# Kernel tuning notes

Measured on AMD Instinct MI355X. Metric: run time of the kernel, lower is better.

The kernel has to match this reference:

```python
import jax, jax.numpy as jnp
import numpy as np

EPS = 0.05      # entropic regularization, matches eps arg in forward
ITERS = 100     # Sinkhorn fixed-point iterations (auction analog; converged math)

def setup_inputs() -> dict:
    key = jax.random.key(0)
    k1, k2 = jax.random.split(key)
    B, N, D = 16, 2048, 3
    x = jax.random.uniform(k1, (B, N, D), dtype=jnp.float32)
    y = jax.random.uniform(k2, (B, N, D), dtype=jnp.float32)
    return {"x": x, "y": y}

def _emd_mean(x, y):
    # pairwise squared distances: [B, N, N]
    x2 = jnp.sum(x * x, axis=-1)                      # [B, N]
    y2 = jnp.sum(y * y, axis=-1)                      # [B, N]
    xy = jnp.einsum('bnd,bmd->bnm', x, y)             # [B, N, N]
    C = x2[:, :, None] + y2[:, None, :] - 2.0 * xy
    C = jnp.maximum(C, 0.0)

    B, N, _ = C.shape
    logK = -C / EPS                                   # [B, N, N]
    log_mu = jnp.full((B, N), -jnp.log(jnp.float32(N)))
    log_nu = log_mu

    def body(carry, _):
        f, g = carry
        # f_i = eps*(log mu_i - logsumexp_j((g_j - C_ij)/eps))
        f = EPS * (log_mu - jax.nn.logsumexp(logK + (g / EPS)[:, None, :], axis=2))
        g = EPS * (log_nu - jax.nn.logsumexp(logK + (f / EPS)[:, :, None], axis=1))
        return (f, g), None

    f0 = jnp.zeros((B, N), dtype=C.dtype)
    g0 = jnp.zeros((B, N), dtype=C.dtype)
    (f, g), _ = jax.lax.scan(body, (f0, g0), None, length=ITERS)

    # transport plan P_ij = exp((f_i + g_j - C_ij)/eps) (already includes mu,nu)
    logP = (f[:, :, None] + g[:, None, :] - C) / EPS
    P = jnp.exp(logP)
    # per-source-point matched squared distance, scaled by N (row mass = 1/N)
    dis = jnp.sum(P * C, axis=2) * N                  # [B, N]
    return dis.mean()

def reference(x, y):
    return _emd_mean(x, y)
```

## Files before the change

kernel.cpp:

```cpp
#include <hip/hip_runtime.h>

#define BB 16
#define NN 2048
#define NITERS 100

#define K2E      28.853900817779268f
#define TWO_K2E  57.707801635558536f
#define INV2K    0.017328679513998632f
#define INV_K2E  0.034657359027997264f
#define INV4K    0.008664339756999316f
#define LMU      (-11.0f)

#if __has_builtin(__builtin_amdgcn_exp2f)
#define EXP2F(x) __builtin_amdgcn_exp2f(x)
#else
#define EXP2F(x) exp2f(x)
#endif

typedef float v2f __attribute__((ext_vector_type(2)));
typedef float v4f __attribute__((ext_vector_type(4)));

#define DSTORE(p, v) __hip_atomic_store((p), (v), __ATOMIC_RELAXED, __HIP_MEMORY_SCOPE_AGENT)
#define DLOAD(p)     __hip_atomic_load((p), __ATOMIC_RELAXED, __HIP_MEMORY_SCOPE_AGENT)

__device__ __forceinline__ float bfly8(const float acc[8], int lane) {
    const bool b0 = lane & 1, b1 = lane & 2, b2 = lane & 4;
    float v4[4], v2_[2], v1;
    #pragma unroll
    for (int i = 0; i < 4; ++i) {
        float recv = __shfl_xor(b0 ? acc[i] : acc[i+4], 1, 64);
        v4[i] = (b0 ? acc[i+4] : acc[i]) + recv;
    }
    #pragma unroll
    for (int i = 0; i < 2; ++i) {
        float recv = __shfl_xor(b1 ? v4[i] : v4[i+2], 2, 64);
        v2_[i] = (b1 ? v4[i+2] : v4[i]) + recv;
    }
    {
        float recv = __shfl_xor(b2 ? v2_[0] : v2_[1], 4, 64);
        v1 = (b2 ? v2_[1] : v2_[0]) + recv;
    }
    v1 += __shfl_xor(v1, 8, 64);
    v1 += __shfl_xor(v1, 16, 64);
    v1 += __shfl_xor(v1, 32, 64);
    return v1;
}

__device__ __forceinline__ float sumpassF(
    const v4f* __restrict__ U, const v4f* __restrict__ T,
    const float* __restrict__ sdv,
    int rloc, int lane)
{
    v2f xp0[4], xp1[4], xp2[4], acc2[4];
    #pragma unroll
    for (int p = 0; p < 4; ++p) {
        const v4f ua = U[rloc + 2*p];
        const v4f ub = U[rloc + 2*p + 1];
        xp0[p] = (v2f){ua.x * INV2K, ub.x * INV2K};
        xp1[p] = (v2f){ua.y * INV2K, ub.y * INV2K};
        xp2[p] = (v2f){ua.z * INV2K, ub.z * INV2K};
        acc2[p] = (v2f){0.f, 0.f};
    }
    #pragma unroll 4
    for (int s = 0; s < 32; ++s) {
        const int p = lane + (s << 6);
        const v4f t = T[p];
        const float ad = sdv[p];
        const v2f a0v = (v2f){t.x, t.x}, a1v = (v2f){t.y, t.y};
        const v2f a2v = (v2f){t.z, t.z}, adv = (v2f){ad, ad};
        #pragma unroll
        for (int qq = 0; qq < 4; ++qq) {
            v2f d = __builtin_elementwise_fma(xp0[qq], a0v,
                    __builtin_elementwise_fma(xp1[qq], a1v,
                    __builtin_elementwise_fma(xp2[qq], a2v, adv)));
            acc2[qq] += (v2f){EXP2F(d.x), EXP2F(d.y)};
        }
    }
    float acc[8];
    #pragma unroll
    for (int p = 0; p < 4; ++p) { acc[2*p] = acc2[p].x; acc[2*p+1] = acc2[p].y; }
    return bfly8(acc, lane);
}

__device__ __forceinline__ float epilA(
    const v4f* __restrict__ U, const v4f* __restrict__ T,
    const float* __restrict__ gB,
    float Aval, int rloc, int jh, int lane)
{
    const int jb = (jh << 10) + lane;
    float dv[16];
    #pragma unroll
    for (int s = 0; s < 16; ++s)
        dv[s] = DLOAD(gB + jb + (s << 6));

    float xr0[8], xr1[8], xr2[8], Ak[8], x2k[8];
    #pragma unroll
    for (int k = 0; k < 8; ++k) {
        const v4f u = U[rloc + k];
        xr0[k] = u.x * INV2K;
        xr1[k] = u.y * INV2K;
        xr2[k] = u.z * INV2K;
        const int src = ((k & 1) << 2) | (k & 2) | ((k >> 2) & 1);
        Ak[k]  = __shfl(Aval, src, 64);
        x2k[k] = K2E * (xr0[k]*xr0[k] + xr1[k]*xr1[k] + xr2[k]*xr2[k]);
    }
    float acc = 0.f;
    for (int s = 0; s < 16; ++s) {
        const v4f t = T[jb + (s << 6)];
        const float a0 = t.x, a1 = t.y, a2 = t.z, tb = dv[s];
        const float q2 = (a0*a0 + a1*a1 + a2*a2) * INV4K;
        #pragma unroll
        for (int k = 0; k < 8; ++k) {
            float d = fmaf(xr0[k], a0, fmaf(xr1[k], a1, fmaf(xr2[k], a2, tb)));
            float P = EXP2F(d + Ak[k]);
            float C = fmaxf((x2k[k] + q2 - (d - tb)) * INV_K2E, 0.f);
            acc = fmaf(P, C, acc);
        }
    }
    return acc;
}

__global__ __launch_bounds__(512, 4) void emd_sinkhornV(
    const float* __restrict__ x, const float* __restrict__ y,
    float* __restrict__ Af, float* __restrict__ Bf,
    int* __restrict__ flags, float* __restrict__ out)
{
    extern __shared__ float S[];
    __shared__ float wsum[8];

    const int tid  = threadIdx.x;
    const int lane = tid & 63;
    const int w    = tid >> 6;
    const int blk  = blockIdx.x;
    const int b    = blk >> 5;
    const int q    = blk & 31;
    const int base = b * NN;
    const int row0 = q * 64;
    const int rloc = row0 + w * 8;
    int* fb = flags + b * 128;

    v4f   *sy = (v4f*)S;
    v4f   *sx = (v4f*)S + NN;
    float *sd = (float*)((v4f*)S + 2 * NN);

    #pragma unroll
    for (int v = 0; v < 4; ++v) {
        const int p = tid + (v << 9);
        const float* px = x + 3 * (size_t)(base + p);
        sx[p] = (v4f){TWO_K2E * px[0], TWO_K2E * px[1], TWO_K2E * px[2], 0.f};
        const float* py = y + 3 * (size_t)(base + p);
        sy[p] = (v4f){TWO_K2E * py[0], TWO_K2E * py[1], TWO_K2E * py[2], 0.f};
    }
    if (tid < 64) {
        const int col = row0 + tid;
        const float* py = y + 3 * (size_t)(base + col);
        const float a = py[0], bb = py[1], c = py[2];
        DSTORE(&Bf[base + col], -K2E * (a*a + bb*bb + c*c));
    }
    __syncthreads();
    if (tid == 0)
        __hip_atomic_store(fb + q * 4, 1, __ATOMIC_RELEASE, __HIP_MEMORY_SCOPE_AGENT);

    #define WAITB(tgt) do { __syncthreads();                                    \
        if (w == 0) {                                                           \
            for (;;) {                                                          \
                int vv = (lane < 32)                                            \
                    ? __hip_atomic_load(fb + lane * 4, __ATOMIC_RELAXED,        \
                                        __HIP_MEMORY_SCOPE_AGENT)               \
                    : 0x7fffffff;                                               \
                if (__ballot(vv >= (tgt)) == ~0ULL) break;                      \
                __builtin_amdgcn_s_sleep(1);                                    \
            }                                                                   \
        }                                                                       \
        __syncthreads(); } while (0)

    #define POSTB(pval) do { __syncthreads();                                   \
        if (tid == 0)                                                           \
            __hip_atomic_store(fb + q * 4, (pval), __ATOMIC_RELEASE,            \
                               __HIP_MEMORY_SCOPE_AGENT);                       \
    } while (0)

    #define STAGE(gsrc) do {                                                    \
        float t0_ = DLOAD((gsrc) + tid);                                        \
        float t1_ = DLOAD((gsrc) + tid + 512);                                  \
        float t2_ = DLOAD((gsrc) + tid + 1024);                                 \
        float t3_ = DLOAD((gsrc) + tid + 1536);                                 \
        sd[tid] = t0_; sd[tid + 512] = t1_;                                     \
        sd[tid + 1024] = t2_; sd[tid + 1536] = t3_;                             \
        __syncthreads(); } while (0)

    WAITB(1);

    const int rr = ((lane & 1) << 2) | (lane & 2) | ((lane >> 2) & 1);
    float Aval = 0.f;

    for (int it = 0; it < NITERS; ++it) {
        STAGE(Bf + base);
        {
            float v1 = sumpassF(sx, sy, sd, rloc, lane);
            Aval = LMU - __log2f(v1);
            if (lane < 8) DSTORE(&Af[base + rloc + rr], Aval);
        }
        POSTB(2 * it + 2);
        WAITB(2 * it + 2);
        STAGE(Af + base);
        {
            float v1 = sumpassF(sy, sx, sd, rloc, lane);
            if (lane < 8)
                DSTORE(&Bf[base + rloc + rr], LMU - __log2f(v1));
        }
        POSTB(2 * it + 3);
        WAITB(2 * it + 3);
    }

    {
        float s = epilA(sx, sy, Bf + base, Aval, rloc, 0, lane)
                + epilA(sx, sy, Bf + base, Aval, rloc, 1, lane);
        #pragma unroll
        for (int m = 32; m > 0; m >>= 1) s += __shfl_xor(s, m, 64);
        if (lane == 0) wsum[w] = s;
        __syncthreads();
        if (tid == 0) {
            float t = 0.f;
            #pragma unroll
            for (int i = 0; i < 8; ++i) t += wsum[i];
            atomicAdd(out, t * (1.0f / (float)BB));
        }
    }
    #undef WAITB
    #undef POSTB
    #undef STAGE
}

__global__ __launch_bounds__(1024, 4) void emd_sinkhornU(
    const float* __restrict__ x, const float* __restrict__ y,
    float* __restrict__ Af, float* __restrict__ Bf,
    int* __restrict__ flags, float* __restrict__ out)
{
    extern __shared__ float S[];
    __shared__ float wsum[16];

    const int tid  = threadIdx.x;
    const int lane = tid & 63;
    const int w    = tid >> 6;
    const int blk  = blockIdx.x;
    const int b    = blk >> 4;
    const int q    = blk & 15;
    const int base = b * NN;
    const int row0 = q * 128;
    const int rloc = row0 + w * 8;
    int* fb = flags + 2048 + b * 64;

    v4f   *sy = (v4f*)S;
    v4f   *sx = (v4f*)S + NN;
    float *sd = (float*)((v4f*)S + 2 * NN);

    #pragma unroll
    for (int v = 0; v < 2; ++v) {
        const int p = tid + (v << 10);
        const float* px = x + 3 * (size_t)(base + p);
        sx[p] = (v4f){TWO_K2E * px[0], TWO_K2E * px[1], TWO_K2E * px[2], 0.f};
        const float* py = y + 3 * (size_t)(base + p);
        sy[p] = (v4f){TWO_K2E * py[0], TWO_K2E * py[1], TWO_K2E * py[2], 0.f};
    }
    if (tid < 128) {
        const int col = row0 + tid;
        const float* py = y + 3 * (size_t)(base + col);
        const float a = py[0], bb = py[1], c = py[2];
        DSTORE(&Bf[base + col], -K2E * (a*a + bb*bb + c*c));
    }
    __syncthreads();
    if (tid == 0)
        __hip_atomic_store(fb + q * 4, 1, __ATOMIC_RELEASE, __HIP_MEMORY_SCOPE_AGENT);

    #define WAITB2(tgt) do { __syncthreads();                                   \
        if (w == 0) {                                                           \
            for (;;) {                                                          \
                int vv = (lane < 16)                                            \
                    ? __hip_atomic_load(fb + lane * 4, __ATOMIC_RELAXED,        \
                                        __HIP_MEMORY_SCOPE_AGENT)               \
                    : 0x7fffffff;                                               \
                if (__ballot(vv >= (tgt)) == ~0ULL) break;                      \
                __builtin_amdgcn_s_sleep(1);                                    \
            }                                                                   \
        }                                                                       \
        __syncthreads(); } while (0)

    #define POSTB2(pval) do { __syncthreads();                                  \
        if (tid == 0)                                                           \
            __hip_atomic_store(fb + q * 4, (pval), __ATOMIC_RELEASE,            \
                               __HIP_MEMORY_SCOPE_AGENT);                       \
    } while (0)

    #define STAGE2(gsrc) do {                                                   \
        float t0_ = DLOAD((gsrc) + tid);                                        \
        float t1_ = DLOAD((gsrc) + tid + 1024);                                 \
        sd[tid] = t0_; sd[tid + 1024] = t1_;                                    \
        __syncthreads(); } while (0)

    WAITB2(1);

    const int rr = ((lane & 1) << 2) | (lane & 2) | ((lane >> 2) & 1);
    float Aval = 0.f;

    for (int it = 0; it < NITERS; ++it) {
        STAGE2(Bf + base);
        {
            float v1 = sumpassF(sx, sy, sd, rloc, lane);
            Aval = LMU - __log2f(v1);
            if (lane < 8) DSTORE(&Af[base + rloc + rr], Aval);
        }
        POSTB2(2 * it + 2);
        WAITB2(2 * it + 2);
        STAGE2(Af + base);
        {
            float v1 = sumpassF(sy, sx, sd, rloc, lane);
            if (lane < 8)
                DSTORE(&Bf[base + rloc + rr], LMU - __log2f(v1));
        }
        POSTB2(2 * it + 3);
        WAITB2(2 * it + 3);
    }

    {
        float s = epilA(sx, sy, Bf + base, Aval, rloc, 0, lane)
                + epilA(sx, sy, Bf + base, Aval, rloc, 1, lane);
        #pragma unroll
        for (int m = 32; m > 0; m >>= 1) s += __shfl_xor(s, m, 64);
        if (lane == 0) wsum[w] = s;
        __syncthreads();
        if (tid == 0) {
            float t = 0.f;
            #pragma unroll
            for (int i = 0; i < 16; ++i) t += wsum[i];
            atomicAdd(out, t * (1.0f / (float)BB));
        }
    }
    #undef WAITB2
    #undef POSTB2
    #undef STAGE2
}

extern "C" void kernel_launch(void* const* d_in, const int* in_sizes, int n_in,
                              void* d_out, int out_size, void* d_ws, size_t ws_size,
                              hipStream_t stream) {
    const float* x = (const float*)d_in[0];
    const float* y = (const float*)d_in[1];
    float* out = (float*)d_out;
    char* ws = (char*)d_ws;

    int*   flags = (int*)ws;
    float* Af    = (float*)(ws + 16384);
    float* Bf    = (float*)(ws + 16384 + (size_t)BB*NN*sizeof(float));

    hipMemsetAsync(flags, 0, 16384, stream);
    hipMemsetAsync(out, 0, sizeof(float), stream);

    void* args[] = {(void*)&x, (void*)&y, (void*)&Af, (void*)&Bf,
                    (void*)&flags, (void*)&out};

    const size_t shmem = (size_t)(2 * NN * 4 + NN) * sizeof(float);
    hipError_t ev = hipFuncSetAttribute((const void*)emd_sinkhornV,
                        hipFuncAttributeMaxDynamicSharedMemorySize, (int)shmem);
    hipError_t e = (ev == hipSuccess)
        ? hipLaunchCooperativeKernel((const void*)emd_sinkhornV,
                                     dim3(512), dim3(512), args, shmem, stream)
        : hipErrorInvalidValue;
    if (e != hipSuccess) {
        hipError_t eu = hipFuncSetAttribute((const void*)emd_sinkhornU,
                            hipFuncAttributeMaxDynamicSharedMemorySize, (int)shmem);
        hipError_t e2 = (eu == hipSuccess)
            ? hipLaunchCooperativeKernel((const void*)emd_sinkhornU,
                                         dim3(256), dim3(1024), args, shmem, stream)
            : hipErrorInvalidValue;
        if (e2 != hipSuccess) {
            hipLaunchKernelGGL(emd_sinkhornU, dim3(256), dim3(1024), shmem,
                               stream, x, y, Af, Bf, flags, out);
        }
    }
}
```

Baseline: 2.496 ms.

## Use 1024-thread blocks with fused per-wave flag polling and staging barrier

Replaces the 512-block, 512-thread cooperative kernel with 256 blocks of 1024 threads, which halves the number of blocks per batch that must meet at each grid-wide flag barrier. The separate post, wait and stage steps are merged into one macro. Every wave now polls the 16 per-batch flags itself and then stages its own slice of the dual vector, which removes one __syncthreads and the wave-0 gating per phase. The cost is more concurrent flag polling from all waves, and one large block per CU instead of two smaller ones.

Measured after the change: 2.528 ms. Within noise of the previous version (+1.3%).

```diff
diff --git a/kernel.cpp b/kernel.cpp
--- a/kernel.cpp
+++ b/kernel.cpp
@@ -120,97 +120,84 @@
     return acc;
 }
 
-__global__ __launch_bounds__(512, 4) void emd_sinkhornV(
+__global__ __launch_bounds__(1024, 4) void emd_sinkhornP(
     const float* __restrict__ x, const float* __restrict__ y,
     float* __restrict__ Af, float* __restrict__ Bf,
     int* __restrict__ flags, float* __restrict__ out)
 {
     extern __shared__ float S[];
-    __shared__ float wsum[8];
+    __shared__ float wsum[16];
 
     const int tid  = threadIdx.x;
     const int lane = tid & 63;
     const int w    = tid >> 6;
     const int blk  = blockIdx.x;
-    const int b    = blk >> 5;
-    const int q    = blk & 31;
+    const int b    = blk >> 4;
+    const int q    = blk & 15;
     const int base = b * NN;
-    const int row0 = q * 64;
+    const int row0 = q * 128;
     const int rloc = row0 + w * 8;
-    int* fb = flags + b * 128;
+    int* fb = flags + b * 64;
 
     v4f   *sy = (v4f*)S;
     v4f   *sx = (v4f*)S + NN;
     float *sd = (float*)((v4f*)S + 2 * NN);
 
     #pragma unroll
-    for (int v = 0; v < 4; ++v) {
-        const int p = tid + (v << 9);
+    for (int v = 0; v < 2; ++v) {
+        const int p = tid + (v << 10);
         const float* px = x + 3 * (size_t)(base + p);
         sx[p] = (v4f){TWO_K2E * px[0], TWO_K2E * px[1], TWO_K2E * px[2], 0.f};
         const float* py = y + 3 * (size_t)(base + p);
         sy[p] = (v4f){TWO_K2E * py[0], TWO_K2E * py[1], TWO_K2E * py[2], 0.f};
     }
-    if (tid < 64) {
+    if (tid < 128) {
         const int col = row0 + tid;
         const float* py = y + 3 * (size_t)(base + col);
         const float a = py[0], bb = py[1], c = py[2];
         DSTORE(&Bf[base + col], -K2E * (a*a + bb*bb + c*c));
     }
-    __syncthreads();
-    if (tid == 0)
-        __hip_atomic_store(fb + q * 4, 1, __ATOMIC_RELEASE, __HIP_MEMORY_SCOPE_AGENT);
-
-    #define WAITB(tgt) do { __syncthreads();                                    \
-        if (w == 0) {                                                           \
-            for (;;) {                                                          \
-                int vv = (lane < 32)                                            \
-                    ? __hip_atomic_load(fb + lane * 4, __ATOMIC_RELAXED,        \
-                                        __HIP_MEMORY_SCOPE_AGENT)               \
-                    : 0x7fffffff;                                               \
-                if (__ballot(vv >= (tgt)) == ~0ULL) break;                      \
-                __builtin_amdgcn_s_sleep(1);                                    \
-            }                                                                   \
-        }                                                                       \
-        __syncthreads(); } while (0)
-
-    #define POSTB(pval) do { __syncthreads();                                   \
+
+    #define PWS(pval, tgt, gsrc) do {                                           \
+        __syncthreads();          \
         if (tid == 0)                                                           \
             __hip_atomic_store(fb + q * 4, (pval), __ATOMIC_RELEASE,            \
                                __HIP_MEMORY_SCOPE_AGENT);                       \
+        for (;;) {                                                              \
+            int vv = (lane < 16)                                                \
+                ? __hip_atomic_load(fb + lane * 4, __ATOMIC_RELAXED,            \
+                                    __HIP_MEMORY_SCOPE_AGENT)                   \
+                : 0x7fffffff;                                                   \
+            if (__ballot(vv >= (tgt)) == ~0ULL) break;                          \
+            __builtin_amdgcn_s_sleep(1);                                        \
+        }                                                                       \
+        {                                   \
+            const int o_ = (w << 7) + lane;                                     \
+            float a_ = DLOAD((gsrc) + o_);                                      \
+            float b_ = DLOAD((gsrc) + o_ + 64);                                 \
+            sd[o_] = a_; sd[o_ + 64] = b_;                                      \
+        }                                                                       \
+        __syncthreads();                                       \
     } while (0)
-
-    #define STAGE(gsrc) do {                                                    \
-        float t0_ = DLOAD((gsrc) + tid);                                        \
-        float t1_ = DLOAD((gsrc) + tid + 512);                                  \
-        float t2_ = DLOAD((gsrc) + tid + 1024);                                 \
-        float t3_ = DLOAD((gsrc) + tid + 1536);                                 \
-        sd[tid] = t0_; sd[tid + 512] = t1_;                                     \
-        sd[tid + 1024] = t2_; sd[tid + 1536] = t3_;                             \
-        __syncthreads(); } while (0)
-
-    WAITB(1);
 
     const int rr = ((lane & 1) << 2) | (lane & 2) | ((lane >> 2) & 1);
     float Aval = 0.f;
 
+    PWS(1, 1, Bf + base);
+
     for (int it = 0; it < NITERS; ++it) {
-        STAGE(Bf + base);
         {
             float v1 = sumpassF(sx, sy, sd, rloc, lane);
             Aval = LMU - __log2f(v1);
             if (lane < 8) DSTORE(&Af[base + rloc + rr], Aval);
         }
-        POSTB(2 * it + 2);
-        WAITB(2 * it + 2);
-        STAGE(Af + base);
+        PWS(2 * it + 2, 2 * it + 2, Af + base);
         {
             float v1 = sumpassF(sy, sx, sd, rloc, lane);
             if (lane < 8)
                 DSTORE(&Bf[base + rloc + rr], LMU - __log2f(v1));
         }
-        POSTB(2 * it + 3);
-        WAITB(2 * it + 3);
+        PWS(2 * it + 3, 2 * it + 3, Bf + base);
     }
 
     {
@@ -223,13 +210,11 @@
         if (tid == 0) {
             float t = 0.f;
             #pragma unroll
-            for (int i = 0; i < 8; ++i) t += wsum[i];
+            for (int i = 0; i < 16; ++i) t += wsum[i];
             atomicAdd(out, t * (1.0f / (float)BB));
         }
     }
-    #undef WAITB
-    #undef POSTB
-    #undef STAGE
+    #undef PWS
 }
 
 __global__ __launch_bounds__(1024, 4) void emd_sinkhornU(
@@ -360,11 +345,11 @@
                     (void*)&flags, (void*)&out};
 
     const size_t shmem = (size_t)(2 * NN * 4 + NN) * sizeof(float);
-    hipError_t ev = hipFuncSetAttribute((const void*)emd_sinkhornV,
+    hipError_t ep = hipFuncSetAttribute((const void*)emd_sinkhornP,
                         hipFuncAttributeMaxDynamicSharedMemorySize, (int)shmem);
-    hipError_t e = (ev == hipSuccess)
-        ? hipLaunchCooperativeKernel((const void*)emd_sinkhornV,
-                                     dim3(512), dim3(512), args, shmem, stream)
+    hipError_t e = (ep == hipSuccess)
+        ? hipLaunchCooperativeKernel((const void*)emd_sinkhornP,
+                                     dim3(256), dim3(1024), args, shmem, stream)
         : hipErrorInvalidValue;
     if (e != hipSuccess) {
         hipError_t eu = hipFuncSetAttribute((const void*)emd_sinkhornU,
```
